# Kernel optimization log

Hardware: AMD Instinct MI355X
Metric: run time of the kernel (lower is better)

Reference implementation:

```python
import jax, jax.numpy as jnp
import numpy as np

N = 100000      # nodes
E = 1600000     # edges (avg degree 16)
F_IN = 64       # node_features_size
C1, C2 = 32, 64 # conv out channels (heads=1)
H1, NC = 128, 10


def setup_inputs() -> dict:
    key = jax.random.key(0)
    ks = jax.random.split(key, 24)
    g = lambda k, shape, s=0.1: (jax.random.normal(k, shape, jnp.float32) * s)
    inp = {
        "x": jax.random.normal(ks[0], (N, F_IN), jnp.float32),
        "edge_index": jax.random.randint(ks[1], (2, E), 0, N, jnp.int32),
        "edge_attr": jax.random.normal(ks[2], (E, 1), jnp.float32),
        # conv1 params (query/key/value/edge/skip), weights stored [in, out]
        "Wq1": g(ks[3], (F_IN, C1)), "bq1": jnp.zeros((C1,), jnp.float32),
        "Wk1": g(ks[4], (F_IN, C1)), "bk1": jnp.zeros((C1,), jnp.float32),
        "Wv1": g(ks[5], (F_IN, C1)), "bv1": jnp.zeros((C1,), jnp.float32),
        "We1": g(ks[6], (1, C1)),    "be1": jnp.zeros((C1,), jnp.float32),
        "Ws1": g(ks[7], (F_IN, C1)), "bs1": jnp.zeros((C1,), jnp.float32),
        # conv2 params
        "Wq2": g(ks[8], (C1, C2)),  "bq2": jnp.zeros((C2,), jnp.float32),
        "Wk2": g(ks[9], (C1, C2)),  "bk2": jnp.zeros((C2,), jnp.float32),
        "Wv2": g(ks[10], (C1, C2)), "bv2": jnp.zeros((C2,), jnp.float32),
        "We2": g(ks[11], (1, C2)),  "be2": jnp.zeros((C2,), jnp.float32),
        "Ws2": g(ks[12], (C1, C2)), "bs2": jnp.zeros((C2,), jnp.float32),
        # MLP head
        "W_fc1": g(ks[13], (C2, H1)), "b_fc1": jnp.zeros((H1,), jnp.float32),
        "W_fc2": g(ks[14], (H1, NC)), "b_fc2": jnp.zeros((NC,), jnp.float32),
    }
    return inp


def transformer_conv(x, src, dst, edge_attr, Wq, bq, Wk, bk, Wv, bv, We, be, Ws, bs):
    # PyG TransformerConv, heads=1, concat=True, root_weight=True, beta=False
    C = Wq.shape[1]
    q = x @ Wq + bq                       # [N, C]
    k = x @ Wk + bk                       # [N, C]
    v = x @ Wv + bv                       # [N, C]
    e = edge_attr @ We + be               # [E, C]
    ke = k[src] + e                       # [E, C]
    ve = v[src] + e                       # [E, C]
    alpha = jnp.sum(q[dst] * ke, axis=-1) / jnp.sqrt(jnp.float32(C))  # [E]
    # segment softmax over incoming edges of each target node
    m = jax.ops.segment_max(alpha, dst, num_segments=x.shape[0])
    a = jnp.exp(alpha - m[dst])
    s = jax.ops.segment_sum(a, dst, num_segments=x.shape[0])
    a = a / (s[dst] + 1e-16)
    out = jax.ops.segment_sum(a[:, None] * ve, dst, num_segments=x.shape[0])  # [N, C]
    return out + (x @ Ws + bs)            # root/skip connection


def reference(x, edge_index, edge_attr,
              Wq1, bq1, Wk1, bk1, Wv1, bv1, We1, be1, Ws1, bs1,
              Wq2, bq2, Wk2, bk2, Wv2, bv2, We2, be2, Ws2, bs2,
              W_fc1, b_fc1, W_fc2, b_fc2):
    src, dst = edge_index[0], edge_index[1]
    h = jax.nn.elu(transformer_conv(x, src, dst, edge_attr,
                                    Wq1, bq1, Wk1, bk1, Wv1, bv1, We1, be1, Ws1, bs1))
    h = jax.nn.elu(transformer_conv(h, src, dst, edge_attr,
                                    Wq2, bq2, Wk2, bk2, Wv2, bv2, We2, be2, Ws2, bs2))
    h = jax.nn.elu(h @ W_fc1 + b_fc1)
    logits = h @ W_fc2 + b_fc2
    return jax.nn.log_softmax(logits, axis=1)
```

## Files before the change

kernel.cpp:

```cpp
#include <hip/hip_runtime.h>
#include <hip/hip_fp16.h>
#include <math.h>


#define SCAN_NB 256

typedef _Float16 half8 __attribute__((ext_vector_type(8)));
typedef float f32x4 __attribute__((ext_vector_type(4)));

__global__ __launch_bounds__(256)
void count_rank_kernel(const int* __restrict__ dst, int* __restrict__ deg,
                       int* __restrict__ rank, int e) {
    for (int i = blockIdx.x * 256 + threadIdx.x; i < e; i += gridDim.x * 256)
        rank[i] = atomicAdd(deg + dst[i], 1);
}

__global__ __launch_bounds__(256)
void blocksum_kernel(const int* __restrict__ deg, int* __restrict__ bsum, int n) {
    __shared__ int ls[256];
    const int chunk = (n + gridDim.x - 1) / gridDim.x;
    const int b0 = blockIdx.x * chunk;
    const int b1 = (b0 + chunk < n) ? b0 + chunk : n;
    int s = 0;
    for (int i = b0 + threadIdx.x; i < b1; i += 256) s += deg[i];
    ls[threadIdx.x] = s;
    __syncthreads();
    for (int off = 128; off > 0; off >>= 1) {
        if (threadIdx.x < off) ls[threadIdx.x] += ls[threadIdx.x + off];
        __syncthreads();
    }
    if (threadIdx.x == 0) bsum[blockIdx.x] = ls[0];
}

__global__ __launch_bounds__(256)
void scanb_kernel(const int* __restrict__ bsum, int* __restrict__ boff,
                  int* __restrict__ total, int nb) {
    __shared__ int ls[256];
    const int t = threadIdx.x;
    int v = (t < nb) ? bsum[t] : 0;
    ls[t] = v;
    __syncthreads();
    for (int off = 1; off < 256; off <<= 1) {
        int u = (t >= off) ? ls[t - off] : 0;
        __syncthreads();
        ls[t] += u;
        __syncthreads();
    }
    if (t < nb) boff[t] = ls[t] - v;
    if (t == 255) *total = ls[255];
}

__global__ __launch_bounds__(256)
void writeptr_kernel(const int* __restrict__ deg, const int* __restrict__ boff,
                     int* __restrict__ rowptr, int n) {
    __shared__ int ls[256];
    const int chunk = (n + gridDim.x - 1) / gridDim.x;
    const int b0 = blockIdx.x * chunk;
    const int b1 = (b0 + chunk < n) ? b0 + chunk : n;
    const int tchunk = (chunk + 255) / 256;
    const int t0 = b0 + threadIdx.x * tchunk;
    const int t1 = (t0 + tchunk < b1) ? t0 + tchunk : b1;
    int s = 0;
    for (int i = t0; i < t1; ++i) s += deg[i];
    ls[threadIdx.x] = s;
    __syncthreads();
    for (int off = 1; off < 256; off <<= 1) {
        int u = (threadIdx.x >= off) ? ls[threadIdx.x - off] : 0;
        __syncthreads();
        ls[threadIdx.x] += u;
        __syncthreads();
    }
    int run = boff[blockIdx.x] + ls[threadIdx.x] - s;
    for (int i = t0; i < t1; ++i) { rowptr[i] = run; run += deg[i]; }
}

__global__ __launch_bounds__(256)
void fill_pack_kernel(const int* __restrict__ src, const int* __restrict__ dst,
                      const float* __restrict__ eattr,
                      const int* __restrict__ rowptr, const int* __restrict__ rank,
                      int2* __restrict__ ecsr, int e) {
    for (int i = blockIdx.x * 256 + threadIdx.x; i < e; i += gridDim.x * 256) {
        int p = rowptr[dst[i]] + rank[i];
        ecsr[p] = make_int2(src[i], __float_as_int(eattr[i]));
    }
}

template<int FIN, int C>
__global__ __launch_bounds__(256, 2)
void linear4_mfma_kernel(const float* __restrict__ X,
                         const float* __restrict__ Wq, const float* __restrict__ bq,
                         const float* __restrict__ Wk, const float* __restrict__ bk,
                         const float* __restrict__ Wv, const float* __restrict__ bv,
                         const float* __restrict__ Ws, const float* __restrict__ bs,
                         float* __restrict__ q, __half2* __restrict__ kv,
                         float* __restrict__ s, int n)
{
    constexpr int FOURC = 4 * C;
    constexpr int P  = FIN + 16;
    constexpr int KT = FIN / 32;
    constexpr int NT = FOURC / 16;
    __shared__ _Float16 wsh[FOURC * P] __attribute__((aligned(16)));
    __shared__ float bsh[FOURC];

    for (int i = threadIdx.x; i < FOURC * FIN; i += 256) {
        int col = i / FIN, f = i - (i / FIN) * FIN;
        float w;
        if (col < C)          w = Wq[f * C + col];
        else if (col < 2 * C) w = Ws[f * C + col - C];
        else if (col < 3 * C) w = Wk[f * C + col - 2 * C];
        else                  w = Wv[f * C + col - 3 * C];
        wsh[col * P + f] = (_Float16)w;
    }
    for (int i = threadIdx.x; i < FOURC; i += 256) {
        bsh[i] = (i < C) ? bq[i] : (i < 2 * C) ? bs[i - C]
               : (i < 3 * C) ? bk[i - 2 * C] : bv[i - 3 * C];
    }
    __syncthreads();

    const int lane = threadIdx.x & 63;
    const int wid  = threadIdx.x >> 6;
    const int m = lane & 15, g = lane >> 4;

    half8 bfrag[KT][NT];
    #pragma unroll
    for (int kt = 0; kt < KT; ++kt)
        #pragma unroll
        for (int nt = 0; nt < NT; ++nt)
            bfrag[kt][nt] = *reinterpret_cast<const half8*>(
                &wsh[(nt * 16 + m) * P + kt * 32 + g * 8]);

    const int tiles = n >> 4;
    for (int t = blockIdx.x * 4 + wid; t < tiles; t += gridDim.x * 4) {
        const int row0 = t * 16;
        const float* xr = X + (size_t)(row0 + m) * FIN + g * 8;
        half8 afrag[KT];
        #pragma unroll
        for (int kt = 0; kt < KT; ++kt) {
            float4 u = *reinterpret_cast<const float4*>(xr + kt * 32);
            float4 w = *reinterpret_cast<const float4*>(xr + kt * 32 + 4);
            afrag[kt] = half8{(_Float16)u.x, (_Float16)u.y, (_Float16)u.z, (_Float16)u.w,
                              (_Float16)w.x, (_Float16)w.y, (_Float16)w.z, (_Float16)w.w};
        }
        #pragma unroll
        for (int nt = 0; nt < 2 * C / 16; ++nt) {
            f32x4 acc = {0.f, 0.f, 0.f, 0.f};
            #pragma unroll
            for (int kt = 0; kt < KT; ++kt)
                acc = __builtin_amdgcn_mfma_f32_16x16x32_f16(afrag[kt], bfrag[kt][nt], acc, 0, 0, 0);
            const int col = nt * 16 + m;
            const float bias = bsh[col];
            float* outp = (nt < C / 16) ? q : s;
            const int cc = (nt < C / 16) ? col : col - C;
            #pragma unroll
            for (int r = 0; r < 4; ++r)
                outp[(size_t)(row0 + g * 4 + r) * C + cc] = acc[r] + bias;
        }
        #pragma unroll
        for (int t2 = 0; t2 < C / 16; ++t2) {
            const int ntK = 2 * C / 16 + t2, ntV = 3 * C / 16 + t2;
            f32x4 aK = {0.f, 0.f, 0.f, 0.f}, aV = {0.f, 0.f, 0.f, 0.f};
            #pragma unroll
            for (int kt = 0; kt < KT; ++kt) {
                aK = __builtin_amdgcn_mfma_f32_16x16x32_f16(afrag[kt], bfrag[kt][ntK], aK, 0, 0, 0);
                aV = __builtin_amdgcn_mfma_f32_16x16x32_f16(afrag[kt], bfrag[kt][ntV], aV, 0, 0, 0);
            }
            const int ck = t2 * 16 + m;
            const float bK = bsh[2 * C + ck], bV = bsh[3 * C + ck];
            #pragma unroll
            for (int r = 0; r < 4; ++r)
                kv[(size_t)(row0 + g * 4 + r) * C + ck] = __floats2half2_rn(aK[r] + bK, aV[r] + bV);
        }
    }
}

template<int FIN, int COUT>
__global__ __launch_bounds__(256, 2)
void linear_mfma_kernel(const float* __restrict__ X, const float* __restrict__ W,
                        const float* __restrict__ b, float* __restrict__ out, int n)
{
    constexpr int P  = FIN + 16;
    constexpr int KT = FIN / 32;
    constexpr int NT = COUT / 16;
    __shared__ _Float16 wsh[COUT * P] __attribute__((aligned(16)));
    __shared__ float bsh[COUT];
    for (int i = threadIdx.x; i < COUT * FIN; i += 256) {
        int col = i / FIN, f = i - (i / FIN) * FIN;
        wsh[col * P + f] = (_Float16)W[f * COUT + col];
    }
    for (int i = threadIdx.x; i < COUT; i += 256) bsh[i] = b[i];
    __syncthreads();

    const int lane = threadIdx.x & 63;
    const int wid  = threadIdx.x >> 6;
    const int m = lane & 15, g = lane >> 4;

    half8 bfrag[KT][NT];
    #pragma unroll
    for (int kt = 0; kt < KT; ++kt)
        #pragma unroll
        for (int nt = 0; nt < NT; ++nt)
            bfrag[kt][nt] = *reinterpret_cast<const half8*>(
                &wsh[(nt * 16 + m) * P + kt * 32 + g * 8]);

    const int tiles = n >> 4;
    for (int t = blockIdx.x * 4 + wid; t < tiles; t += gridDim.x * 4) {
        const int row0 = t * 16;
        const float* xr = X + (size_t)(row0 + m) * FIN + g * 8;
        half8 afrag[KT];
        #pragma unroll
        for (int kt = 0; kt < KT; ++kt) {
            float4 u = *reinterpret_cast<const float4*>(xr + kt * 32);
            float4 w = *reinterpret_cast<const float4*>(xr + kt * 32 + 4);
            afrag[kt] = half8{(_Float16)u.x, (_Float16)u.y, (_Float16)u.z, (_Float16)u.w,
                              (_Float16)w.x, (_Float16)w.y, (_Float16)w.z, (_Float16)w.w};
        }
        #pragma unroll
        for (int nt = 0; nt < NT; ++nt) {
            f32x4 acc = {0.f, 0.f, 0.f, 0.f};
            #pragma unroll
            for (int kt = 0; kt < KT; ++kt)
                acc = __builtin_amdgcn_mfma_f32_16x16x32_f16(afrag[kt], bfrag[kt][nt], acc, 0, 0, 0);
            const int col = nt * 16 + m;
            const float bias = bsh[col];
            #pragma unroll
            for (int r = 0; r < 4; ++r) {
                float hv = acc[r] + bias;
                hv = (hv > 0.f) ? hv : expm1f(hv);
                out[(size_t)(row0 + g * 4 + r) * COUT + col] = hv;
            }
        }
    }
}

template<int C>
__global__ __launch_bounds__(256)
void conv_fused_kernel(const int* __restrict__ rowptr, const int2* __restrict__ ecsr,
                       const float* __restrict__ q, const __half2* __restrict__ kv,
                       const float* __restrict__ sres,
                       const float* __restrict__ We, const float* __restrict__ be,
                       float* __restrict__ h, float scale, int n)
{
    constexpr int LPE    = C / 4;
    constexpr int EPI    = 64 / LPE;
    constexpr int LOG    = (C == 64) ? 4 : 3;
    constexpr int UNROLL = (C == 64) ? 4 : 2;
    const int wave = threadIdx.x >> 6;
    const int lane = threadIdx.x & 63;
    const int l    = lane & (LPE - 1);
    const int slot = lane >> LOG;
    const int c0   = 4 * l;
    const int node = blockIdx.x * 4 + wave;
    if (node >= n) return;

    const float4 wec = *reinterpret_cast<const float4*>(We + c0);
    const float4 bec = *reinterpret_cast<const float4*>(be + c0);
    const float4 qp  = *reinterpret_cast<const float4*>(q + (size_t)node * C + c0);
    const int r0 = rowptr[node], r1 = rowptr[node + 1];

    float pd1 = fmaf(qp.x, wec.x, fmaf(qp.y, wec.y, fmaf(qp.z, wec.z, qp.w * wec.w)));
    float pd0 = fmaf(qp.x, bec.x, fmaf(qp.y, bec.y, fmaf(qp.z, bec.z, qp.w * bec.w)));
    #pragma unroll
    for (int off = LPE >> 1; off > 0; off >>= 1) {
        pd1 += __shfl_xor(pd1, off);
        pd0 += __shfl_xor(pd0, off);
    }
    const float sd1 = pd1 * scale, sd0 = pd0 * scale;

    float ssum = 0.f, swea = 0.f;
    float a0 = 0.f, a1 = 0.f, a2 = 0.f, a3 = 0.f;
    const int j0 = r0 + slot;
    const int iters = (r1 - j0 + EPI - 1) / EPI;
    for (int it = 0; it < iters; it += UNROLL) {
        int2 epk[UNROLL]; float4 kvr[UNROLL]; bool ok[UNROLL];
        #pragma unroll
        for (int u = 0; u < UNROLL; ++u) {
            int j = j0 + (it + u) * EPI;
            ok[u] = j < r1;
            epk[u] = ecsr[ok[u] ? j : r0];
        }
        #pragma unroll
        for (int u = 0; u < UNROLL; ++u)
            kvr[u] = *reinterpret_cast<const float4*>(kv + (size_t)epk[u].x * C + c0);
        #pragma unroll
        for (int u = 0; u < UNROLL; ++u) {
            float ea = __int_as_float(epk[u].y);
            float2 f0 = __half22float2(*reinterpret_cast<__half2*>(&kvr[u].x));
            float2 f1 = __half22float2(*reinterpret_cast<__half2*>(&kvr[u].y));
            float2 f2 = __half22float2(*reinterpret_cast<__half2*>(&kvr[u].z));
            float2 f3 = __half22float2(*reinterpret_cast<__half2*>(&kvr[u].w));
            float p = fmaf(qp.x, f0.x, fmaf(qp.y, f1.x, fmaf(qp.z, f2.x, qp.w * f3.x)));
            #pragma unroll
            for (int off = LPE >> 1; off > 0; off >>= 1) p += __shfl_xor(p, off);
            float w = __expf(fmaf(scale, p, fmaf(sd1, ea, sd0)));
            w = ok[u] ? w : 0.f;
            ssum += w;
            swea = fmaf(w, ea, swea);
            a0 = fmaf(w, f0.y, a0);
            a1 = fmaf(w, f1.y, a1);
            a2 = fmaf(w, f2.y, a2);
            a3 = fmaf(w, f3.y, a3);
        }
    }

    #pragma unroll
    for (int off = LPE; off < 64; off <<= 1) {
        ssum += __shfl_xor(ssum, off);
        swea += __shfl_xor(swea, off);
        a0   += __shfl_xor(a0, off);
        a1   += __shfl_xor(a1, off);
        a2   += __shfl_xor(a2, off);
        a3   += __shfl_xor(a3, off);
    }

    if (slot == 0) {
        float inv = 1.f / (ssum + 1e-16f);
        float t0 = fmaf(wec.x, swea, fmaf(bec.x, ssum, a0));
        float t1 = fmaf(wec.y, swea, fmaf(bec.y, ssum, a1));
        float t2 = fmaf(wec.z, swea, fmaf(bec.z, ssum, a2));
        float t3 = fmaf(wec.w, swea, fmaf(bec.w, ssum, a3));
        float4 sr = *reinterpret_cast<const float4*>(sres + (size_t)node * C + c0);
        float h0 = fmaf(t0, inv, sr.x);
        float h1 = fmaf(t1, inv, sr.y);
        float h2v = fmaf(t2, inv, sr.z);
        float h3 = fmaf(t3, inv, sr.w);
        h0 = (h0 > 0.f) ? h0 : expm1f(h0);
        h1 = (h1 > 0.f) ? h1 : expm1f(h1);
        h2v = (h2v > 0.f) ? h2v : expm1f(h2v);
        h3 = (h3 > 0.f) ? h3 : expm1f(h3);
        *reinterpret_cast<float4*>(h + (size_t)node * C + c0) = make_float4(h0, h1, h2v, h3);
    }
}

#define H1_DIM 128
#define NC_DIM 10
__global__ __launch_bounds__(256)
void head_kernel(const float* __restrict__ Hf, const float* __restrict__ W,
                 const float* __restrict__ b, float* __restrict__ out, int n)
{
    __shared__ float wsh[H1_DIM * NC_DIM];
    __shared__ float bsh[NC_DIM];
    for (int i = threadIdx.x; i < H1_DIM * NC_DIM; i += 256) wsh[i] = W[i];
    for (int i = threadIdx.x; i < NC_DIM; i += 256) bsh[i] = b[i];
    __syncthreads();
    for (int row = blockIdx.x * 256 + threadIdx.x; row < n; row += gridDim.x * 256) {
        const float* hr = Hf + (size_t)row * H1_DIM;
        float logit[NC_DIM];
        #pragma unroll
        for (int c = 0; c < NC_DIM; ++c) logit[c] = bsh[c];
        for (int f = 0; f < H1_DIM; ++f) {
            float xv = hr[f];
            #pragma unroll
            for (int c = 0; c < NC_DIM; ++c) logit[c] = fmaf(xv, wsh[f * NC_DIM + c], logit[c]);
        }
        float m = logit[0];
        #pragma unroll
        for (int c = 1; c < NC_DIM; ++c) m = fmaxf(m, logit[c]);
        float sum = 0.f;
        #pragma unroll
        for (int c = 0; c < NC_DIM; ++c) sum += __expf(logit[c] - m);
        float lse = m + logf(sum);
        #pragma unroll
        for (int c = 0; c < NC_DIM; ++c) out[(size_t)row * NC_DIM + c] = logit[c] - lse;
    }
}

extern "C" void kernel_launch(void* const* d_in, const int* in_sizes, int n_in,
                              void* d_out, int out_size, void* d_ws, size_t ws_size,
                              hipStream_t stream) {
    const float* x   = (const float*)d_in[0];
    const int*   ei  = (const int*)d_in[1];
    const float* ea  = (const float*)d_in[2];
    const float *Wq1 = (const float*)d_in[3],  *bq1 = (const float*)d_in[4];
    const float *Wk1 = (const float*)d_in[5],  *bk1 = (const float*)d_in[6];
    const float *Wv1 = (const float*)d_in[7],  *bv1 = (const float*)d_in[8];
    const float *We1 = (const float*)d_in[9],  *be1 = (const float*)d_in[10];
    const float *Ws1 = (const float*)d_in[11], *bs1 = (const float*)d_in[12];
    const float *Wq2 = (const float*)d_in[13], *bq2 = (const float*)d_in[14];
    const float *Wk2 = (const float*)d_in[15], *bk2 = (const float*)d_in[16];
    const float *Wv2 = (const float*)d_in[17], *bv2 = (const float*)d_in[18];
    const float *We2 = (const float*)d_in[19], *be2 = (const float*)d_in[20];
    const float *Ws2 = (const float*)d_in[21], *bs2 = (const float*)d_in[22];
    const float *Wf1 = (const float*)d_in[23], *bf1 = (const float*)d_in[24];
    const float *Wf2 = (const float*)d_in[25], *bf2 = (const float*)d_in[26];

    const int N = in_sizes[0] / 64;
    const int E = in_sizes[2];
    const int* src = ei;
    const int* dst = ei + E;

    float* wsf = (float*)d_ws;
    const size_t N64 = (size_t)N * 64;
    float* q      = wsf;
    __half2* kv   = (__half2*)(q + N64);
    float* s      = (float*)(kv + N64);
    float* h1     = s + N64;
    float* h2     = h1 + (size_t)N * 32;
    int* deg      = (int*)(h2 + N64);
    int* rowptr   = deg + N;
    int* bsum     = rowptr + N + 1;
    int* boff     = bsum + SCAN_NB;
    int* rank     = boff + SCAN_NB;
    int2* ecsr    = (int2*)(rank + E);
    float* hfc    = wsf;

    float* out = (float*)d_out;

    hipMemsetAsync(deg, 0, (size_t)N * 4, stream);
    count_rank_kernel<<<2048, 256, 0, stream>>>(dst, deg, rank, E);
    blocksum_kernel<<<SCAN_NB, 256, 0, stream>>>(deg, bsum, N);
    scanb_kernel<<<1, 256, 0, stream>>>(bsum, boff, rowptr + N, SCAN_NB);
    writeptr_kernel<<<SCAN_NB, 256, 0, stream>>>(deg, boff, rowptr, N);
    fill_pack_kernel<<<4096, 256, 0, stream>>>(src, dst, ea, rowptr, rank, ecsr, E);

    const int convGrid = (N + 3) / 4;

    linear4_mfma_kernel<64, 32><<<1024, 256, 0, stream>>>(
        x, Wq1, bq1, Wk1, bk1, Wv1, bv1, Ws1, bs1, q, kv, s, N);
    conv_fused_kernel<32><<<convGrid, 256, 0, stream>>>(
        rowptr, ecsr, q, kv, s, We1, be1, h1, 0.17677669529663687f, N);

    linear4_mfma_kernel<32, 64><<<1024, 256, 0, stream>>>(
        h1, Wq2, bq2, Wk2, bk2, Wv2, bv2, Ws2, bs2, q, kv, s, N);
    conv_fused_kernel<64><<<convGrid, 256, 0, stream>>>(
        rowptr, ecsr, q, kv, s, We2, be2, h2, 0.125f, N);

    linear_mfma_kernel<64, 128><<<1024, 256, 0, stream>>>(h2, Wf1, bf1, hfc, N);
    head_kernel<<<512, 256, 0, stream>>>(hfc, Wf2, bf2, out, N);
}
```

Measured before the change: 337.7 us.

## Co-schedule degree counting with first linear and fuse MLP head

Merges the atomic degree-count kernel and the first-layer QKVS projection into one launch, with blocks split by role (two count blocks per linear block) so the latency-bound atomics overlap with MFMA work. Separately fuses the fc1 MFMA + ELU with the fc2 projection and log-softmax, keeping the 128-wide hidden activations in registers and reducing across lanes with shuffles instead of writing and rereading an N×128 buffer. Risks include role-split load imbalance, higher register pressure from the per-row partial sums, and extra shuffle traffic.

```diff
diff --git a/kernel.cpp b/kernel.cpp
--- a/kernel.cpp
+++ b/kernel.cpp
@@ -7,13 +7,6 @@
 
 typedef _Float16 half8 __attribute__((ext_vector_type(8)));
 typedef float f32x4 __attribute__((ext_vector_type(4)));
-
-__global__ __launch_bounds__(256)
-void count_rank_kernel(const int* __restrict__ dst, int* __restrict__ deg,
-                       int* __restrict__ rank, int e) {
-    for (int i = blockIdx.x * 256 + threadIdx.x; i < e; i += gridDim.x * 256)
-        rank[i] = atomicAdd(deg + dst[i], 1);
-}
 
 __global__ __launch_bounds__(256)
 void blocksum_kernel(const int* __restrict__ deg, int* __restrict__ bsum, int n) {
@@ -85,6 +78,107 @@
     }
 }
 
+#define CNT_NB 2048
+#define L4_NB  1024
+template<int FIN, int C>
+__global__ __launch_bounds__(256, 2)
+void count_linear4_kernel(const int* __restrict__ dst, int* __restrict__ deg,
+                          int* __restrict__ rank, int e,
+                          const float* __restrict__ X,
+                          const float* __restrict__ Wq, const float* __restrict__ bq,
+                          const float* __restrict__ Wk, const float* __restrict__ bk,
+                          const float* __restrict__ Wv, const float* __restrict__ bv,
+                          const float* __restrict__ Ws, const float* __restrict__ bs,
+                          float* __restrict__ q, __half2* __restrict__ kv,
+                          float* __restrict__ s, int n)
+{
+    constexpr int FOURC = 4 * C;
+    constexpr int P  = FIN + 16;
+    constexpr int KT = FIN / 32;
+    constexpr int NT = FOURC / 16;
+    __shared__ _Float16 wsh[FOURC * P] __attribute__((aligned(16)));
+    __shared__ float bsh[FOURC];
+
+    const int b3 = blockIdx.x / 3, role = blockIdx.x % 3;
+    if (role < 2) {
+        const int cb = b3 * 2 + role;
+        for (int i = cb * 256 + threadIdx.x; i < e; i += CNT_NB * 256)
+            rank[i] = atomicAdd(deg + dst[i], 1);
+        return;
+    }
+
+    const int lb = b3;
+    for (int i = threadIdx.x; i < FOURC * FIN; i += 256) {
+        int col = i / FIN, f = i - (i / FIN) * FIN;
+        float w;
+        if (col < C)          w = Wq[f * C + col];
+        else if (col < 2 * C) w = Ws[f * C + col - C];
+        else if (col < 3 * C) w = Wk[f * C + col - 2 * C];
+        else                  w = Wv[f * C + col - 3 * C];
+        wsh[col * P + f] = (_Float16)w;
+    }
+    for (int i = threadIdx.x; i < FOURC; i += 256) {
+        bsh[i] = (i < C) ? bq[i] : (i < 2 * C) ? bs[i - C]
+               : (i < 3 * C) ? bk[i - 2 * C] : bv[i - 3 * C];
+    }
+    __syncthreads();
+
+    const int lane = threadIdx.x & 63;
+    const int wid  = threadIdx.x >> 6;
+    const int m = lane & 15, g = lane >> 4;
+
+    half8 bfrag[KT][NT];
+    #pragma unroll
+    for (int kt = 0; kt < KT; ++kt)
+        #pragma unroll
+        for (int nt = 0; nt < NT; ++nt)
+            bfrag[kt][nt] = *reinterpret_cast<const half8*>(
+                &wsh[(nt * 16 + m) * P + kt * 32 + g * 8]);
+
+    const int tiles = n >> 4;
+    for (int t = lb * 4 + wid; t < tiles; t += L4_NB * 4) {
+        const int row0 = t * 16;
+        const float* xr = X + (size_t)(row0 + m) * FIN + g * 8;
+        half8 afrag[KT];
+        #pragma unroll
+        for (int kt = 0; kt < KT; ++kt) {
+            float4 u = *reinterpret_cast<const float4*>(xr + kt * 32);
+            float4 w = *reinterpret_cast<const float4*>(xr + kt * 32 + 4);
+            afrag[kt] = half8{(_Float16)u.x, (_Float16)u.y, (_Float16)u.z, (_Float16)u.w,
+                              (_Float16)w.x, (_Float16)w.y, (_Float16)w.z, (_Float16)w.w};
+        }
+        #pragma unroll
+        for (int nt = 0; nt < 2 * C / 16; ++nt) {
+            f32x4 acc = {0.f, 0.f, 0.f, 0.f};
+            #pragma unroll
+            for (int kt = 0; kt < KT; ++kt)
+                acc = __builtin_amdgcn_mfma_f32_16x16x32_f16(afrag[kt], bfrag[kt][nt], acc, 0, 0, 0);
+            const int col = nt * 16 + m;
+            const float bias = bsh[col];
+            float* outp = (nt < C / 16) ? q : s;
+            const int cc = (nt < C / 16) ? col : col - C;
+            #pragma unroll
+            for (int r = 0; r < 4; ++r)
+                outp[(size_t)(row0 + g * 4 + r) * C + cc] = acc[r] + bias;
+        }
+        #pragma unroll
+        for (int t2 = 0; t2 < C / 16; ++t2) {
+            const int ntK = 2 * C / 16 + t2, ntV = 3 * C / 16 + t2;
+            f32x4 aK = {0.f, 0.f, 0.f, 0.f}, aV = {0.f, 0.f, 0.f, 0.f};
+            #pragma unroll
+            for (int kt = 0; kt < KT; ++kt) {
+                aK = __builtin_amdgcn_mfma_f32_16x16x32_f16(afrag[kt], bfrag[kt][ntK], aK, 0, 0, 0);
+                aV = __builtin_amdgcn_mfma_f32_16x16x32_f16(afrag[kt], bfrag[kt][ntV], aV, 0, 0, 0);
+            }
+            const int ck = t2 * 16 + m;
+            const float bK = bsh[2 * C + ck], bV = bsh[3 * C + ck];
+            #pragma unroll
+            for (int r = 0; r < 4; ++r)
+                kv[(size_t)(row0 + g * 4 + r) * C + ck] = __floats2half2_rn(aK[r] + bK, aV[r] + bV);
+        }
+    }
+}
+
 template<int FIN, int C>
 __global__ __launch_bounds__(256, 2)
 void linear4_mfma_kernel(const float* __restrict__ X,
@@ -169,65 +263,6 @@
             #pragma unroll
             for (int r = 0; r < 4; ++r)
                 kv[(size_t)(row0 + g * 4 + r) * C + ck] = __floats2half2_rn(aK[r] + bK, aV[r] + bV);
-        }
-    }
-}
-
-template<int FIN, int COUT>
-__global__ __launch_bounds__(256, 2)
-void linear_mfma_kernel(const float* __restrict__ X, const float* __restrict__ W,
-                        const float* __restrict__ b, float* __restrict__ out, int n)
-{
-    constexpr int P  = FIN + 16;
-    constexpr int KT = FIN / 32;
-    constexpr int NT = COUT / 16;
-    __shared__ _Float16 wsh[COUT * P] __attribute__((aligned(16)));
-    __shared__ float bsh[COUT];
-    for (int i = threadIdx.x; i < COUT * FIN; i += 256) {
-        int col = i / FIN, f = i - (i / FIN) * FIN;
-        wsh[col * P + f] = (_Float16)W[f * COUT + col];
-    }
-    for (int i = threadIdx.x; i < COUT; i += 256) bsh[i] = b[i];
-    __syncthreads();
-
-    const int lane = threadIdx.x & 63;
-    const int wid  = threadIdx.x >> 6;
-    const int m = lane & 15, g = lane >> 4;
-
-    half8 bfrag[KT][NT];
-    #pragma unroll
-    for (int kt = 0; kt < KT; ++kt)
-        #pragma unroll
-        for (int nt = 0; nt < NT; ++nt)
-            bfrag[kt][nt] = *reinterpret_cast<const half8*>(
-                &wsh[(nt * 16 + m) * P + kt * 32 + g * 8]);
-
-    const int tiles = n >> 4;
-    for (int t = blockIdx.x * 4 + wid; t < tiles; t += gridDim.x * 4) {
-        const int row0 = t * 16;
-        const float* xr = X + (size_t)(row0 + m) * FIN + g * 8;
-        half8 afrag[KT];
-        #pragma unroll
-        for (int kt = 0; kt < KT; ++kt) {
-            float4 u = *reinterpret_cast<const float4*>(xr + kt * 32);
-            float4 w = *reinterpret_cast<const float4*>(xr + kt * 32 + 4);
-            afrag[kt] = half8{(_Float16)u.x, (_Float16)u.y, (_Float16)u.z, (_Float16)u.w,
-                              (_Float16)w.x, (_Float16)w.y, (_Float16)w.z, (_Float16)w.w};
-        }
-        #pragma unroll
-        for (int nt = 0; nt < NT; ++nt) {
-            f32x4 acc = {0.f, 0.f, 0.f, 0.f};
-            #pragma unroll
-            for (int kt = 0; kt < KT; ++kt)
-                acc = __builtin_amdgcn_mfma_f32_16x16x32_f16(afrag[kt], bfrag[kt][nt], acc, 0, 0, 0);
-            const int col = nt * 16 + m;
-            const float bias = bsh[col];
-            #pragma unroll
-            for (int r = 0; r < 4; ++r) {
-                float hv = acc[r] + bias;
-                hv = (hv > 0.f) ? hv : expm1f(hv);
-                out[(size_t)(row0 + g * 4 + r) * COUT + col] = hv;
-            }
         }
     }
 }
@@ -331,36 +366,107 @@
     }
 }
 
-#define H1_DIM 128
-#define NC_DIM 10
-__global__ __launch_bounds__(256)
-void head_kernel(const float* __restrict__ Hf, const float* __restrict__ W,
-                 const float* __restrict__ b, float* __restrict__ out, int n)
+template<int FIN, int COUT, int NCLS>
+__global__ __launch_bounds__(256, 2)
+void linear_head_mfma_kernel(const float* __restrict__ X,
+                             const float* __restrict__ W1, const float* __restrict__ b1,
+                             const float* __restrict__ W2, const float* __restrict__ b2,
+                             float* __restrict__ out, int n)
 {
-    __shared__ float wsh[H1_DIM * NC_DIM];
-    __shared__ float bsh[NC_DIM];
-    for (int i = threadIdx.x; i < H1_DIM * NC_DIM; i += 256) wsh[i] = W[i];
-    for (int i = threadIdx.x; i < NC_DIM; i += 256) bsh[i] = b[i];
+    constexpr int P  = FIN + 16;
+    constexpr int KT = FIN / 32;
+    constexpr int NT = COUT / 16;
+    __shared__ _Float16 wsh[COUT * P] __attribute__((aligned(16)));
+    __shared__ float bsh[COUT];
+    __shared__ float w2sh[COUT * NCLS];
+    __shared__ float b2sh[NCLS];
+    for (int i = threadIdx.x; i < COUT * FIN; i += 256) {
+        int col = i / FIN, f = i - (i / FIN) * FIN;
+        wsh[col * P + f] = (_Float16)W1[f * COUT + col];
+    }
+    for (int i = threadIdx.x; i < COUT; i += 256) bsh[i] = b1[i];
+    for (int i = threadIdx.x; i < COUT * NCLS; i += 256) w2sh[i] = W2[i];
+    for (int i = threadIdx.x; i < NCLS; i += 256) b2sh[i] = b2[i];
     __syncthreads();
-    for (int row = blockIdx.x * 256 + threadIdx.x; row < n; row += gridDim.x * 256) {
-        const float* hr = Hf + (size_t)row * H1_DIM;
-        float logit[NC_DIM];
-        #pragma unroll
-        for (int c = 0; c < NC_DIM; ++c) logit[c] = bsh[c];
-        for (int f = 0; f < H1_DIM; ++f) {
-            float xv = hr[f];
-            #pragma unroll
-            for (int c = 0; c < NC_DIM; ++c) logit[c] = fmaf(xv, wsh[f * NC_DIM + c], logit[c]);
-        }
-        float m = logit[0];
-        #pragma unroll
-        for (int c = 1; c < NC_DIM; ++c) m = fmaxf(m, logit[c]);
-        float sum = 0.f;
-        #pragma unroll
-        for (int c = 0; c < NC_DIM; ++c) sum += __expf(logit[c] - m);
-        float lse = m + logf(sum);
-        #pragma unroll
-        for (int c = 0; c < NC_DIM; ++c) out[(size_t)row * NC_DIM + c] = logit[c] - lse;
+
+    const int lane = threadIdx.x & 63;
+    const int wid  = threadIdx.x >> 6;
+    const int m = lane & 15, g = lane >> 4;
+
+    half8 bfrag[KT][NT];
+    #pragma unroll
+    for (int kt = 0; kt < KT; ++kt)
+        #pragma unroll
+        for (int nt = 0; nt < NT; ++nt)
+            bfrag[kt][nt] = *reinterpret_cast<const half8*>(
+                &wsh[(nt * 16 + m) * P + kt * 32 + g * 8]);
+
+    const int tiles = n >> 4;
+    for (int t = blockIdx.x * 4 + wid; t < tiles; t += gridDim.x * 4) {
+        const int row0 = t * 16;
+        const float* xr = X + (size_t)(row0 + m) * FIN + g * 8;
+        half8 afrag[KT];
+        #pragma unroll
+        for (int kt = 0; kt < KT; ++kt) {
+            float4 u = *reinterpret_cast<const float4*>(xr + kt * 32);
+            float4 w = *reinterpret_cast<const float4*>(xr + kt * 32 + 4);
+            afrag[kt] = half8{(_Float16)u.x, (_Float16)u.y, (_Float16)u.z, (_Float16)u.w,
+                              (_Float16)w.x, (_Float16)w.y, (_Float16)w.z, (_Float16)w.w};
+        }
+        float hv[NT][4];
+        #pragma unroll
+        for (int nt = 0; nt < NT; ++nt) {
+            f32x4 acc = {0.f, 0.f, 0.f, 0.f};
+            #pragma unroll
+            for (int kt = 0; kt < KT; ++kt)
+                acc = __builtin_amdgcn_mfma_f32_16x16x32_f16(afrag[kt], bfrag[kt][nt], acc, 0, 0, 0);
+            const float bias = bsh[nt * 16 + m];
+            #pragma unroll
+            for (int r = 0; r < 4; ++r) {
+                float v = acc[r] + bias;
+                hv[nt][r] = (v > 0.f) ? v : expm1f(v);
+            }
+        }
+        float part[4][NCLS];
+        #pragma unroll
+        for (int r = 0; r < 4; ++r)
+            #pragma unroll
+            for (int c = 0; c < NCLS; ++c) part[r][c] = 0.f;
+        #pragma unroll
+        for (int nt = 0; nt < NT; ++nt) {
+            float w2r[NCLS];
+            #pragma unroll
+            for (int c = 0; c < NCLS; ++c) w2r[c] = w2sh[(nt * 16 + m) * NCLS + c];
+            #pragma unroll
+            for (int r = 0; r < 4; ++r)
+                #pragma unroll
+                for (int c = 0; c < NCLS; ++c)
+                    part[r][c] = fmaf(hv[nt][r], w2r[c], part[r][c]);
+        }
+        #pragma unroll
+        for (int off = 1; off < 16; off <<= 1)
+            #pragma unroll
+            for (int r = 0; r < 4; ++r)
+                #pragma unroll
+                for (int c = 0; c < NCLS; ++c)
+                    part[r][c] += __shfl_xor(part[r][c], off);
+        if (m < 4) {
+            const int r = m;
+            const int row = row0 + g * 4 + r;
+            float logit[NCLS];
+            #pragma unroll
+            for (int c = 0; c < NCLS; ++c) logit[c] = part[r][c] + b2sh[c];
+            float mx = logit[0];
+            #pragma unroll
+            for (int c = 1; c < NCLS; ++c) mx = fmaxf(mx, logit[c]);
+            float sum = 0.f;
+            #pragma unroll
+            for (int c = 0; c < NCLS; ++c) sum += __expf(logit[c] - mx);
+            float lse = mx + logf(sum);
+            #pragma unroll
+            for (int c = 0; c < NCLS; ++c)
+                out[(size_t)row * NCLS + c] = logit[c] - lse;
+        }
     }
 }
 
@@ -401,12 +507,13 @@
     int* boff     = bsum + SCAN_NB;
     int* rank     = boff + SCAN_NB;
     int2* ecsr    = (int2*)(rank + E);
-    float* hfc    = wsf;
 
     float* out = (float*)d_out;
 
     hipMemsetAsync(deg, 0, (size_t)N * 4, stream);
-    count_rank_kernel<<<2048, 256, 0, stream>>>(dst, deg, rank, E);
+    count_linear4_kernel<64, 32><<<CNT_NB / 2 * 3, 256, 0, stream>>>(
+        dst, deg, rank, E,
+        x, Wq1, bq1, Wk1, bk1, Wv1, bv1, Ws1, bs1, q, kv, s, N);
     blocksum_kernel<<<SCAN_NB, 256, 0, stream>>>(deg, bsum, N);
     scanb_kernel<<<1, 256, 0, stream>>>(bsum, boff, rowptr + N, SCAN_NB);
     writeptr_kernel<<<SCAN_NB, 256, 0, stream>>>(deg, boff, rowptr, N);
@@ -414,8 +521,6 @@
 
     const int convGrid = (N + 3) / 4;
 
-    linear4_mfma_kernel<64, 32><<<1024, 256, 0, stream>>>(
-        x, Wq1, bq1, Wk1, bk1, Wv1, bv1, Ws1, bs1, q, kv, s, N);
     conv_fused_kernel<32><<<convGrid, 256, 0, stream>>>(
         rowptr, ecsr, q, kv, s, We1, be1, h1, 0.17677669529663687f, N);
 
@@ -424,6 +529,6 @@
     conv_fused_kernel<64><<<convGrid, 256, 0, stream>>>(
         rowptr, ecsr, q, kv, s, We2, be2, h2, 0.125f, N);
 
-    linear_mfma_kernel<64, 128><<<1024, 256, 0, stream>>>(h2, Wf1, bf1, hfc, N);
-    head_kernel<<<512, 256, 0, stream>>>(hfc, Wf2, bf2, out, N);
-}
+    linear_head_mfma_kernel<64, 128, 10><<<1024, 256, 0, stream>>>(
+        h2, Wf1, bf1, Wf2, bf2, out, N);
+}
```

After: 321.1 us. 4.9% less time.
